# Kernel optimization log

Hardware: AMD Instinct MI355X
Metric: run time of the kernel (lower is better)

The kernel has to match this reference:

```python
import jax, jax.numpy as jnp
import numpy as np

N = 100000   # nodes
E = 640000   # edges
F = 128      # num_features
D = 128      # dim
G = 128      # graphs in batch
BN_EPS = 1e-5


def setup_inputs() -> dict:
    key = jax.random.key(0)
    ks = jax.random.split(key, 16)
    lin = lambda k, i, o: (jax.random.normal(k, (i, o), jnp.float32) / np.sqrt(i)).astype(jnp.float32)
    inp = {
        "x": jax.random.normal(ks[0], (N, F), jnp.float32),
        "edge_index": jax.random.randint(ks[1], (2, E), 0, N),
        "batch": jnp.sort(jax.random.randint(ks[2], (N,), 0, G)),
        # layer 0: Linear(F,D)-ReLU-Linear(D,D), BN(D)
        "W0a": lin(ks[3], F, D), "b0a": jnp.zeros((D,), jnp.float32),
        "W0b": lin(ks[4], D, D), "b0b": jnp.zeros((D,), jnp.float32),
        "g0": jnp.ones((D,), jnp.float32), "be0": jnp.zeros((D,), jnp.float32),
        # layer 1: Linear(D,D)-ReLU-Linear(D,D), BN(D)
        "W1a": lin(ks[5], D, D), "b1a": jnp.zeros((D,), jnp.float32),
        "W1b": lin(ks[6], D, D), "b1b": jnp.zeros((D,), jnp.float32),
        "g1": jnp.ones((D,), jnp.float32), "be1": jnp.zeros((D,), jnp.float32),
        # layer 2: Linear(D,D)-ReLU-Linear(D,1), BN(1)
        "W2a": lin(ks[7], D, D), "b2a": jnp.zeros((D,), jnp.float32),
        "W2b": lin(ks[8], D, 1), "b2b": jnp.zeros((1,), jnp.float32),
        "g2": jnp.ones((1,), jnp.float32), "be2": jnp.zeros((1,), jnp.float32),
    }
    return inp


def _gin_layer(x, src, dst, Wa, ba, Wb, bb, g, be, relu_out):
    # GINConv (eps=0): h = x + sum_{j in N(i)} x_j, then MLP, then BN (train-mode stats)
    agg = jax.ops.segment_sum(x[src], dst, num_segments=N)
    h = x + agg
    h = jax.nn.relu(h @ Wa + ba) @ Wb + bb
    mu = jnp.mean(h, axis=0)
    var = jnp.mean((h - mu) ** 2, axis=0)  # biased var (torch BN normalization)
    h = (h - mu) * jax.lax.rsqrt(var + BN_EPS) * g + be
    return jax.nn.relu(h) if relu_out else h


def reference(x, edge_index, batch,
              W0a, b0a, W0b, b0b, g0, be0,
              W1a, b1a, W1b, b1b, g1, be1,
              W2a, b2a, W2b, b2b, g2, be2):
    src, dst = edge_index[0], edge_index[1]
    h = _gin_layer(x, src, dst, W0a, b0a, W0b, b0b, g0, be0, True)
    h = _gin_layer(h, src, dst, W1a, b1a, W1b, b1b, g1, be1, True)
    h = _gin_layer(h, src, dst, W2a, b2a, W2b, b2b, g2, be2, False)  # [N,1], no final ReLU
    # segment softmax over graphs, temperature 5.0 (PyG softmax semantics)
    z = h / 5.0
    m = jax.ops.segment_max(z, batch, num_segments=G)
    ez = jnp.exp(z - m[batch])
    s = jax.ops.segment_sum(ez, batch, num_segments=G)
    return ez / (s[batch] + 1e-16)
```

## Files before the change

### kernel.cpp

```cpp
#include <hip/hip_runtime.h>
#include <math.h>

#define NN 100000
#define EE 640000
#define GG 128
#define BN_EPS 1e-5f
#define NBLK 98

typedef __attribute__((ext_vector_type(8))) short short8;
typedef __attribute__((ext_vector_type(4))) float f32x4;


__device__ __forceinline__ short f2bf(float f) {
    unsigned u = __float_as_uint(f);
    u += 0x7fffu + ((u >> 16) & 1);
    return (short)(u >> 16);
}
__device__ __forceinline__ float bf2f(short s) {
    return __uint_as_float(((unsigned)(unsigned short)s) << 16);
}
__device__ __forceinline__ int swz(int row, int chunk) {
    return row * 128 + ((chunk ^ (row & 15)) << 3);
}
__device__ __forceinline__ int swze(int row, int col) {
    return row * 128 + (((col >> 3) ^ (row & 15)) << 3) + (col & 7);
}

__global__ void k_setup(const float* __restrict__ x,
                        const float* __restrict__ W0a, const float* __restrict__ W0b,
                        const float* __restrict__ W1a, const float* __restrict__ W1b,
                        const float* __restrict__ W2a, short* __restrict__ Wt,
                        short* __restrict__ Xbf, int* __restrict__ deg,
                        float* __restrict__ smf) {
    int idx = blockIdx.x * 256 + threadIdx.x;
    if (idx < 81920) {
        int wi = idx >> 14, r = idx & 16383;
        const float* W = (wi == 0) ? W0a : (wi == 1) ? W0b : (wi == 2) ? W1a
                        : (wi == 3) ? W1b : W2a;
        int k = r >> 7, n = r & 127;
        Wt[wi * 16384 + n * 128 + k] = f2bf(W[k * 128 + n]);
    }
    if (idx < NN) deg[idx] = 0;
    if (idx < 4112) smf[idx] = 0.0f;
    if (idx < 1600000) {
        const float4* xr = (const float4*)x + (size_t)idx * 2;
        float4 v0 = xr[0], v1 = xr[1];
        short8 o;
        o[0] = f2bf(v0.x); o[1] = f2bf(v0.y); o[2] = f2bf(v0.z); o[3] = f2bf(v0.w);
        o[4] = f2bf(v1.x); o[5] = f2bf(v1.y); o[6] = f2bf(v1.z); o[7] = f2bf(v1.w);
        *(short8*)(Xbf + (size_t)idx * 8) = o;
    }
}

__global__ void k_hist(const int* __restrict__ ei, int* __restrict__ deg) {
    int e = blockIdx.x * 256 + threadIdx.x;
    if (e < EE) atomicAdd(&deg[ei[EE + e]], 1);
}

__global__ __launch_bounds__(1024) void k_scan1(const int* __restrict__ deg,
                                                int* __restrict__ offs,
                                                int* __restrict__ bsums) {
    __shared__ int sm[1024];
    int t = threadIdx.x;
    int i = blockIdx.x * 1024 + t;
    int v = (i < NN) ? deg[i] : 0;
    sm[t] = v;
    __syncthreads();
    for (int off = 1; off < 1024; off <<= 1) {
        int add = (t >= off) ? sm[t - off] : 0;
        __syncthreads();
        sm[t] += add;
        __syncthreads();
    }
    if (i < NN) offs[i] = sm[t] - v;
    if (t == 1023) bsums[blockIdx.x] = sm[1023];
}

__global__ void k_scan2(int* bsums) {
    __shared__ int sm[128];
    int t = threadIdx.x;
    int v = (t < NBLK) ? bsums[t] : 0;
    sm[t] = v;
    __syncthreads();
    for (int off = 1; off < 128; off <<= 1) {
        int add = (t >= off) ? sm[t - off] : 0;
        __syncthreads();
        sm[t] += add;
        __syncthreads();
    }
    if (t < NBLK) bsums[t] = sm[t] - v;
}

__global__ __launch_bounds__(1024) void k_scan3(int* __restrict__ offs,
                                                const int* __restrict__ bsums,
                                                int* __restrict__ pos) {
    int t = threadIdx.x;
    int i = blockIdx.x * 1024 + t;
    if (i < NN) {
        int o = offs[i] + bsums[blockIdx.x];
        offs[i] = o;
        pos[i] = o;
    }
    if (i == 0) offs[NN] = EE;
}

__global__ void k_fill(const int* __restrict__ ei, int* __restrict__ pos,
                       int* __restrict__ csr) {
    int e = blockIdx.x * 256 + threadIdx.x;
    if (e < EE) {
        int d = ei[EE + e];
        int p = atomicAdd(&pos[d], 1);
        csr[p] = ei[e];
    }
}

template <bool BN>
__global__ void k_gather(const short* __restrict__ h, const int* __restrict__ offs,
                         const int* __restrict__ csr, const float* __restrict__ rep,
                         const float* __restrict__ g, const float* __restrict__ be,
                         short* __restrict__ agg) {
    __shared__ float parS[128], parH[128];
    int t = threadIdx.x;
    if constexpr (BN) {
        if (t < 128) {
            float s = 0.f, ss = 0.f;
#pragma unroll
            for (int r = 0; r < 8; ++r) {
                s += rep[r * 256 + t];
                ss += rep[r * 256 + 128 + t];
            }
            const float inv = 1.0f / (float)NN;
            float mu = s * inv;
            float var = ss * inv - mu * mu;
            float sc = g[t] / sqrtf(var + BN_EPS);
            parS[t] = sc;
            parH[t] = be[t] - mu * sc;
        }
        __syncthreads();
    }
    int tt = blockIdx.x * 256 + t;
    int n = tt >> 4, l = t & 15;
    if (n >= NN) return;
    float sc[8], sh[8];
    if constexpr (BN) {
#pragma unroll
        for (int j = 0; j < 8; ++j) { sc[j] = parS[l * 8 + j]; sh[j] = parH[l * 8 + j]; }
    }
    int j0 = offs[n], j1 = offs[n + 1];
    short8 v = *(const short8*)(h + (size_t)n * 128 + l * 8);
    float f[8];
#pragma unroll
    for (int j = 0; j < 8; ++j)
        f[j] = BN ? fmaxf(fmaf(bf2f(v[j]), sc[j], sh[j]), 0.f) : bf2f(v[j]);
    int j = j0;
    for (; j + 1 < j1; j += 2) {
        int s0 = csr[j], s1 = csr[j + 1];
        short8 w0 = *(const short8*)(h + (size_t)s0 * 128 + l * 8);
        short8 w1 = *(const short8*)(h + (size_t)s1 * 128 + l * 8);
#pragma unroll
        for (int k = 0; k < 8; ++k) {
            if constexpr (BN) {
                f[k] += fmaxf(fmaf(bf2f(w0[k]), sc[k], sh[k]), 0.f);
                f[k] += fmaxf(fmaf(bf2f(w1[k]), sc[k], sh[k]), 0.f);
            } else {
                f[k] += bf2f(w0[k]) + bf2f(w1[k]);
            }
        }
    }
    if (j < j1) {
        int s0 = csr[j];
        short8 w0 = *(const short8*)(h + (size_t)s0 * 128 + l * 8);
#pragma unroll
        for (int k = 0; k < 8; ++k)
            f[k] += BN ? fmaxf(fmaf(bf2f(w0[k]), sc[k], sh[k]), 0.f) : bf2f(w0[k]);
    }
    short8 o;
#pragma unroll
    for (int k = 0; k < 8; ++k) o[k] = f2bf(f[k]);
    *(short8*)(agg + (size_t)n * 128 + l * 8) = o;
}

template <bool SECOND>
__global__ __launch_bounds__(256, 2) void k_mlp(const short* __restrict__ hin,
                                                const short* __restrict__ Wta,
                                                const float* __restrict__ ba,
                                                const short* __restrict__ Wtb,
                                                const float* __restrict__ bb,
                                                short* __restrict__ hout,
                                                float* __restrict__ statsRep,
                                                const float* __restrict__ w2,
                                                const float* __restrict__ b2,
                                                float* __restrict__ z,
                                                float* __restrict__ s2rep) {
    __shared__ short Asb[16384];
    __shared__ short Wsb[16384];
    const int t = threadIdx.x;
    const int row0 = blockIdx.x * 128;
    const int lane = t & 63, wave = t >> 6;
    const int r16 = lane & 15, q = lane >> 4;
    const int rh = wave & 1, ch = wave >> 1;
    const int RA = rh * 64, CB = ch * 64;

    short8 wpre[8];
#pragma unroll
    for (int i = 0; i < 8; ++i) {
        int f = i * 256 + t;
        int r = f >> 4, c8 = f & 15;
        int gr = row0 + r;
        short8 v = {0, 0, 0, 0, 0, 0, 0, 0};
        if (gr < NN) v = *(const short8*)(hin + (size_t)gr * 128 + c8 * 8);
        *(short8*)&Asb[swz(r, c8)] = v;
        *(short8*)&Wsb[swz(r, c8)] = *(const short8*)(Wta + r * 128 + c8 * 8);
        if constexpr (SECOND) wpre[i] = *(const short8*)(Wtb + r * 128 + c8 * 8);
    }
    __syncthreads();

    f32x4 acc[4][4];
#pragma unroll
    for (int rt = 0; rt < 4; ++rt)
#pragma unroll
        for (int ct = 0; ct < 4; ++ct) acc[rt][ct] = (f32x4)0.f;

#pragma unroll
    for (int kk = 0; kk < 4; ++kk) {
        short8 b[4], a[4];
#pragma unroll
        for (int ct = 0; ct < 4; ++ct)
            b[ct] = *(const short8*)&Wsb[swz(CB + ct * 16 + r16, kk * 4 + q)];
#pragma unroll
        for (int rt = 0; rt < 4; ++rt)
            a[rt] = *(const short8*)&Asb[swz(RA + rt * 16 + r16, kk * 4 + q)];
#pragma unroll
        for (int rt = 0; rt < 4; ++rt)
#pragma unroll
            for (int ct = 0; ct < 4; ++ct)
                acc[rt][ct] = __builtin_amdgcn_mfma_f32_16x16x32_bf16(a[rt], b[ct], acc[rt][ct], 0, 0, 0);
    }
    __syncthreads();

    float bav[4];
#pragma unroll
    for (int ct = 0; ct < 4; ++ct) bav[ct] = ba[CB + ct * 16 + r16];
#pragma unroll
    for (int rt = 0; rt < 4; ++rt)
#pragma unroll
        for (int ct = 0; ct < 4; ++ct)
#pragma unroll
            for (int rg = 0; rg < 4; ++rg) {
                float m = fmaxf(acc[rt][ct][rg] + bav[ct], 0.f);
                Asb[swze(RA + rt * 16 + q * 4 + rg, CB + ct * 16 + r16)] = f2bf(m);
            }

    if constexpr (!SECOND) {
        __syncthreads();
        const int l16 = t & 15, rr = t >> 4;
        float4 w0 = ((const float4*)w2)[l16 * 2];
        float4 w1 = ((const float4*)w2)[l16 * 2 + 1];
        float b2v = b2[0];
        float s = 0.f, ss = 0.f;
#pragma unroll
        for (int pass = 0; pass < 8; ++pass) {
            int r = pass * 16 + rr;
            int gr = row0 + r;
            short8 v = *(const short8*)&Asb[swz(r, l16)];
            float p = bf2f(v[0]) * w0.x + bf2f(v[1]) * w0.y + bf2f(v[2]) * w0.z +
                      bf2f(v[3]) * w0.w + bf2f(v[4]) * w1.x + bf2f(v[5]) * w1.y +
                      bf2f(v[6]) * w1.z + bf2f(v[7]) * w1.w;
#pragma unroll
            for (int off = 1; off < 16; off <<= 1) p += __shfl_xor(p, off, 16);
            if (l16 == 0 && gr < NN) {
                float h2 = p + b2v;
                z[gr] = h2;
                s += h2;
                ss += h2 * h2;
            }
        }
        s += __shfl_xor(s, 16); s += __shfl_xor(s, 32);
        ss += __shfl_xor(ss, 16); ss += __shfl_xor(ss, 32);
        float* rsm = (float*)Wsb;
        if ((t & 63) == 0) { rsm[wave * 2] = s; rsm[wave * 2 + 1] = ss; }
        __syncthreads();
        if (t == 0) {
            float S = rsm[0] + rsm[2] + rsm[4] + rsm[6];
            float SS = rsm[1] + rsm[3] + rsm[5] + rsm[7];
            int rp = (blockIdx.x & 7) * 2;
            unsafeAtomicAdd(&s2rep[rp], S);
            unsafeAtomicAdd(&s2rep[rp + 1], SS);
        }
        return;
    } else {
#pragma unroll
        for (int i = 0; i < 8; ++i) {
            int f = i * 256 + t;
            int r = f >> 4, c8 = f & 15;
            *(short8*)&Wsb[swz(r, c8)] = wpre[i];
        }
        __syncthreads();

#pragma unroll
        for (int rt = 0; rt < 4; ++rt)
#pragma unroll
            for (int ct = 0; ct < 4; ++ct) acc[rt][ct] = (f32x4)0.f;

#pragma unroll
        for (int kk = 0; kk < 4; ++kk) {
            short8 b[4], a[4];
#pragma unroll
            for (int ct = 0; ct < 4; ++ct)
                b[ct] = *(const short8*)&Wsb[swz(CB + ct * 16 + r16, kk * 4 + q)];
#pragma unroll
            for (int rt = 0; rt < 4; ++rt)
                a[rt] = *(const short8*)&Asb[swz(RA + rt * 16 + r16, kk * 4 + q)];
#pragma unroll
            for (int rt = 0; rt < 4; ++rt)
#pragma unroll
                for (int ct = 0; ct < 4; ++ct)
                    acc[rt][ct] = __builtin_amdgcn_mfma_f32_16x16x32_bf16(a[rt], b[ct], acc[rt][ct], 0, 0, 0);
        }
        __syncthreads();

        float bbv[4];
#pragma unroll
        for (int ct = 0; ct < 4; ++ct) bbv[ct] = bb[CB + ct * 16 + r16];
        float s[4] = {0.f, 0.f, 0.f, 0.f}, ss[4] = {0.f, 0.f, 0.f, 0.f};
#pragma unroll
        for (int rt = 0; rt < 4; ++rt)
#pragma unroll
            for (int ct = 0; ct < 4; ++ct)
#pragma unroll
                for (int rg = 0; rg < 4; ++rg) {
                    int lr = RA + rt * 16 + q * 4 + rg;
                    int gr = row0 + lr;
                    float hv = acc[rt][ct][rg] + bbv[ct];
                    if (gr < NN) { s[ct] += hv; ss[ct] += hv * hv; }
                    Asb[swze(lr, CB + ct * 16 + r16)] = f2bf(hv);
                }
#pragma unroll
        for (int ct = 0; ct < 4; ++ct) {
            s[ct] += __shfl_xor(s[ct], 16);
            s[ct] += __shfl_xor(s[ct], 32);
            ss[ct] += __shfl_xor(ss[ct], 16);
            ss[ct] += __shfl_xor(ss[ct], 32);
        }
        float* redF = (float*)Wsb;
        if (lane < 16) {
#pragma unroll
            for (int ct = 0; ct < 4; ++ct) {
                int col = CB + ct * 16 + r16;
                redF[rh * 256 + col] = s[ct];
                redF[rh * 256 + 128 + col] = ss[ct];
            }
        }
        __syncthreads();
        {
            float v = redF[t] + redF[256 + t];
            unsafeAtomicAdd(&statsRep[(blockIdx.x & 7) * 256 + t], v);
        }
#pragma unroll
        for (int i = 0; i < 8; ++i) {
            int f = i * 256 + t;
            int r = f >> 4, c8 = f & 15;
            int gr = row0 + r;
            if (gr < NN)
                *(short8*)(hout + (size_t)gr * 128 + c8 * 8) = *(const short8*)&Asb[swz(r, c8)];
        }
    }
}

__device__ __forceinline__ int lbound(const int* __restrict__ b, int val) {
    int lo = 0, hi = NN;
    while (lo < hi) {
        int m = (lo + hi) >> 1;
        if (b[m] < val) lo = m + 1; else hi = m;
    }
    return lo;
}

__global__ void k_softmax(const float* __restrict__ zr, const float* __restrict__ s2rep,
                          const float* __restrict__ g2, const float* __restrict__ be2,
                          const int* __restrict__ batch, float* __restrict__ out) {
    __shared__ float rb[4];
    const int g = blockIdx.x, t = threadIdx.x;
    const int lo = lbound(batch, g), hi = lbound(batch, g + 1);
    float s = 0.f, ssq = 0.f;
#pragma unroll
    for (int i = 0; i < 8; ++i) { s += s2rep[i * 2]; ssq += s2rep[i * 2 + 1]; }
    const float mu = s / (float)NN;
    const float var = ssq / (float)NN - mu * mu;
    const float sc = g2[0] / sqrtf(var + BN_EPS) * 0.2f;
    const float sh = (be2[0] - mu * g2[0] / sqrtf(var + BN_EPS)) * 0.2f;

    float m = -INFINITY;
    for (int i = lo + t; i < hi; i += 256) m = fmaxf(m, fmaf(zr[i], sc, sh));
#pragma unroll
    for (int off = 1; off < 64; off <<= 1) m = fmaxf(m, __shfl_xor(m, off, 64));
    if ((t & 63) == 0) rb[t >> 6] = m;
    __syncthreads();
    float gmax = fmaxf(fmaxf(rb[0], rb[1]), fmaxf(rb[2], rb[3]));
    __syncthreads();

    float sum = 0.f;
    for (int i = lo + t; i < hi; i += 256) {
        float e = expf(fmaf(zr[i], sc, sh) - gmax);
        out[i] = e;
        sum += e;
    }
#pragma unroll
    for (int off = 1; off < 64; off <<= 1) sum += __shfl_xor(sum, off, 64);
    if ((t & 63) == 0) rb[t >> 6] = sum;
    __syncthreads();
    float S = rb[0] + rb[1] + rb[2] + rb[3];
    float inv = 1.0f / (S + 1e-16f);
    for (int i = lo + t; i < hi; i += 256) out[i] *= inv;
}

extern "C" void kernel_launch(void* const* d_in, const int* in_sizes, int n_in,
                              void* d_out, int out_size, void* d_ws, size_t ws_size,
                              hipStream_t stream) {
    const float* x   = (const float*)d_in[0];
    const int* ei    = (const int*)d_in[1];
    const int* batch = (const int*)d_in[2];
    const float *W0a = (const float*)d_in[3],  *b0a = (const float*)d_in[4];
    const float *W0b = (const float*)d_in[5],  *b0b = (const float*)d_in[6];
    const float *g0  = (const float*)d_in[7],  *be0 = (const float*)d_in[8];
    const float *W1a = (const float*)d_in[9],  *b1a = (const float*)d_in[10];
    const float *W1b = (const float*)d_in[11], *b1b = (const float*)d_in[12];
    const float *g1  = (const float*)d_in[13], *be1 = (const float*)d_in[14];
    const float *W2a = (const float*)d_in[15], *b2a = (const float*)d_in[16];
    const float *W2b = (const float*)d_in[17], *b2b = (const float*)d_in[18];
    const float *g2  = (const float*)d_in[19], *be2 = (const float*)d_in[20];
    float* out = (float*)d_out;

    char* wsb = (char*)d_ws;
    short* Abf = (short*)wsb;
    short* Bbf = (short*)(wsb + 25600000);
    float* Zb  = (float*)(wsb + 51200000);
    float* SMf = (float*)(wsb + 51600000);
    float* S0r = SMf;
    float* S1r = SMf + 2048;
    float* S2r = SMf + 4096;
    int* offs  = (int*)(wsb + 51620000);
    int* bsums = (int*)(wsb + 52020004);
    int* csr   = (int*)(wsb + 52020516);
    short* Wt  = (short*)(wsb + 54580544);
    short* Xbf = (short*)(wsb + 54744384);
    int* deg = (int*)wsb;
    int* pos = (int*)(wsb + 400000);

    const int gE   = (EE + 255) / 256;
    const int gG16 = (NN * 16) / 256;
    const int gMlp = (NN + 127) / 128;

    k_setup<<<6250, 256, 0, stream>>>(x, W0a, W0b, W1a, W1b, W2a, Wt, Xbf, deg, SMf);

    k_hist<<<gE, 256, 0, stream>>>(ei, deg);
    k_scan1<<<NBLK, 1024, 0, stream>>>(deg, offs, bsums);
    k_scan2<<<1, 128, 0, stream>>>(bsums);
    k_scan3<<<NBLK, 1024, 0, stream>>>(offs, bsums, pos);
    k_fill<<<gE, 256, 0, stream>>>(ei, pos, csr);

    k_gather<false><<<gG16, 256, 0, stream>>>(Xbf, offs, csr, nullptr, nullptr, nullptr, Abf);
    k_mlp<true><<<gMlp, 256, 0, stream>>>(Abf, Wt, b0a, Wt + 16384, b0b, Abf, S0r,
                                          nullptr, nullptr, nullptr, nullptr);
    k_gather<true><<<gG16, 256, 0, stream>>>(Abf, offs, csr, S0r, g0, be0, Bbf);
    k_mlp<true><<<gMlp, 256, 0, stream>>>(Bbf, Wt + 2 * 16384, b1a, Wt + 3 * 16384, b1b,
                                          Bbf, S1r, nullptr, nullptr, nullptr, nullptr);
    k_gather<true><<<gG16, 256, 0, stream>>>(Bbf, offs, csr, S1r, g1, be1, Abf);
    k_mlp<false><<<gMlp, 256, 0, stream>>>(Abf, Wt + 4 * 16384, b2a, nullptr, nullptr,
                                           nullptr, nullptr, W2b, b2b, Zb, S2r);

    k_softmax<<<GG, 256, 0, stream>>>(Zb, S2r, g2, be2, batch, out);
}
```

Baseline: 388.9 us.

## Read MLP weights straight from global/L2 and unroll gather aggregation by four

The MLP kernel no longer stages the weight matrices in shared memory. MFMA B operands are loaded directly from global memory, which is expected to hit in L2 since every block reuses the same weights. This roughly halves LDS per block, and the launch bounds rise to allow four blocks per CU for more occupancy. The cost is more global/L2 traffic inside the MFMA loop, and a syncthreads is moved so it runs on both paths. Separately, the CSR neighbor-gather loop is unrolled from two to four edges so more row loads are in flight, with a loop handling the leftover edges.

Measured after the change: 454.2 us. +16.8%, slower.

```diff
diff --git a/kernel.cpp b/kernel.cpp
--- a/kernel.cpp
+++ b/kernel.cpp
@@ -153,21 +153,25 @@
     for (int j = 0; j < 8; ++j)
         f[j] = BN ? fmaxf(fmaf(bf2f(v[j]), sc[j], sh[j]), 0.f) : bf2f(v[j]);
     int j = j0;
-    for (; j + 1 < j1; j += 2) {
-        int s0 = csr[j], s1 = csr[j + 1];
+    for (; j + 3 < j1; j += 4) {
+        int s0 = csr[j], s1 = csr[j + 1], s2 = csr[j + 2], s3 = csr[j + 3];
         short8 w0 = *(const short8*)(h + (size_t)s0 * 128 + l * 8);
         short8 w1 = *(const short8*)(h + (size_t)s1 * 128 + l * 8);
+        short8 w2 = *(const short8*)(h + (size_t)s2 * 128 + l * 8);
+        short8 w3 = *(const short8*)(h + (size_t)s3 * 128 + l * 8);
 #pragma unroll
         for (int k = 0; k < 8; ++k) {
             if constexpr (BN) {
-                f[k] += fmaxf(fmaf(bf2f(w0[k]), sc[k], sh[k]), 0.f);
-                f[k] += fmaxf(fmaf(bf2f(w1[k]), sc[k], sh[k]), 0.f);
+                f[k] += fmaxf(fmaf(bf2f(w0[k]), sc[k], sh[k]), 0.f)
+                      + fmaxf(fmaf(bf2f(w1[k]), sc[k], sh[k]), 0.f)
+                      + fmaxf(fmaf(bf2f(w2[k]), sc[k], sh[k]), 0.f)
+                      + fmaxf(fmaf(bf2f(w3[k]), sc[k], sh[k]), 0.f);
             } else {
-                f[k] += bf2f(w0[k]) + bf2f(w1[k]);
+                f[k] += bf2f(w0[k]) + bf2f(w1[k]) + bf2f(w2[k]) + bf2f(w3[k]);
             }
         }
     }
-    if (j < j1) {
+    for (; j < j1; ++j) {
         int s0 = csr[j];
         short8 w0 = *(const short8*)(h + (size_t)s0 * 128 + l * 8);
 #pragma unroll
@@ -181,7 +185,7 @@
 }
 
 template <bool SECOND>
-__global__ __launch_bounds__(256, 2) void k_mlp(const short* __restrict__ hin,
+__global__ __launch_bounds__(256, 4) void k_mlp(const short* __restrict__ hin,
                                                 const short* __restrict__ Wta,
                                                 const float* __restrict__ ba,
                                                 const short* __restrict__ Wtb,
@@ -193,15 +197,15 @@
                                                 float* __restrict__ z,
                                                 float* __restrict__ s2rep) {
     __shared__ short Asb[16384];
-    __shared__ short Wsb[16384];
+    __shared__ float redS[512];
     const int t = threadIdx.x;
     const int row0 = blockIdx.x * 128;
     const int lane = t & 63, wave = t >> 6;
     const int r16 = lane & 15, q = lane >> 4;
+    const int q8 = q * 8;
     const int rh = wave & 1, ch = wave >> 1;
     const int RA = rh * 64, CB = ch * 64;
 
-    short8 wpre[8];
 #pragma unroll
     for (int i = 0; i < 8; ++i) {
         int f = i * 256 + t;
@@ -210,8 +214,6 @@
         short8 v = {0, 0, 0, 0, 0, 0, 0, 0};
         if (gr < NN) v = *(const short8*)(hin + (size_t)gr * 128 + c8 * 8);
         *(short8*)&Asb[swz(r, c8)] = v;
-        *(short8*)&Wsb[swz(r, c8)] = *(const short8*)(Wta + r * 128 + c8 * 8);
-        if constexpr (SECOND) wpre[i] = *(const short8*)(Wtb + r * 128 + c8 * 8);
     }
     __syncthreads();
 
@@ -226,7 +228,7 @@
         short8 b[4], a[4];
 #pragma unroll
         for (int ct = 0; ct < 4; ++ct)
-            b[ct] = *(const short8*)&Wsb[swz(CB + ct * 16 + r16, kk * 4 + q)];
+            b[ct] = *(const short8*)(Wta + (CB + ct * 16 + r16) * 128 + kk * 32 + q8);
 #pragma unroll
         for (int rt = 0; rt < 4; ++rt)
             a[rt] = *(const short8*)&Asb[swz(RA + rt * 16 + r16, kk * 4 + q)];
@@ -250,9 +252,9 @@
                 float m = fmaxf(acc[rt][ct][rg] + bav[ct], 0.f);
                 Asb[swze(RA + rt * 16 + q * 4 + rg, CB + ct * 16 + r16)] = f2bf(m);
             }
+    __syncthreads();
 
     if constexpr (!SECOND) {
-        __syncthreads();
         const int l16 = t & 15, rr = t >> 4;
         float4 w0 = ((const float4*)w2)[l16 * 2];
         float4 w1 = ((const float4*)w2)[l16 * 2 + 1];
@@ -277,12 +279,11 @@
         }
         s += __shfl_xor(s, 16); s += __shfl_xor(s, 32);
         ss += __shfl_xor(ss, 16); ss += __shfl_xor(ss, 32);
-        float* rsm = (float*)Wsb;
-        if ((t & 63) == 0) { rsm[wave * 2] = s; rsm[wave * 2 + 1] = ss; }
+        if ((t & 63) == 0) { redS[wave * 2] = s; redS[wave * 2 + 1] = ss; }
         __syncthreads();
         if (t == 0) {
-            float S = rsm[0] + rsm[2] + rsm[4] + rsm[6];
-            float SS = rsm[1] + rsm[3] + rsm[5] + rsm[7];
+            float S = redS[0] + redS[2] + redS[4] + redS[6];
+            float SS = redS[1] + redS[3] + redS[5] + redS[7];
             int rp = (blockIdx.x & 7) * 2;
             unsafeAtomicAdd(&s2rep[rp], S);
             unsafeAtomicAdd(&s2rep[rp + 1], SS);
@@ -290,14 +291,6 @@
         return;
     } else {
 #pragma unroll
-        for (int i = 0; i < 8; ++i) {
-            int f = i * 256 + t;
-            int r = f >> 4, c8 = f & 15;
-            *(short8*)&Wsb[swz(r, c8)] = wpre[i];
-        }
-        __syncthreads();
-
-#pragma unroll
         for (int rt = 0; rt < 4; ++rt)
 #pragma unroll
             for (int ct = 0; ct < 4; ++ct) acc[rt][ct] = (f32x4)0.f;
@@ -307,7 +300,7 @@
             short8 b[4], a[4];
 #pragma unroll
             for (int ct = 0; ct < 4; ++ct)
-                b[ct] = *(const short8*)&Wsb[swz(CB + ct * 16 + r16, kk * 4 + q)];
+                b[ct] = *(const short8*)(Wtb + (CB + ct * 16 + r16) * 128 + kk * 32 + q8);
 #pragma unroll
             for (int rt = 0; rt < 4; ++rt)
                 a[rt] = *(const short8*)&Asb[swz(RA + rt * 16 + r16, kk * 4 + q)];
@@ -342,18 +335,17 @@
             ss[ct] += __shfl_xor(ss[ct], 16);
             ss[ct] += __shfl_xor(ss[ct], 32);
         }
-        float* redF = (float*)Wsb;
         if (lane < 16) {
 #pragma unroll
             for (int ct = 0; ct < 4; ++ct) {
                 int col = CB + ct * 16 + r16;
-                redF[rh * 256 + col] = s[ct];
-                redF[rh * 256 + 128 + col] = ss[ct];
+                redS[rh * 256 + col] = s[ct];
+                redS[rh * 256 + 128 + col] = ss[ct];
             }
         }
         __syncthreads();
         {
-            float v = redF[t] + redF[256 + t];
+            float v = redS[t] + redS[256 + t];
             unsafeAtomicAdd(&statsRep[(blockIdx.x & 7) * 256 + t], v);
         }
 #pragma unroll
```
